# Kernel optimization log

Hardware: AMD Instinct MI355X
Metric: run time of the kernel (lower is better)

The kernel has to match this reference:

```python
import jax, jax.numpy as jnp
import numpy as np

TOTAL_LABELS = 81
MAX_TOTAL_SIZE = 200
SCORE_THRESHOLD = 0.7
IOU_THRESHOLD = 0.5  # tf.image.combined_non_max_suppression default
VARIANCES = jnp.array([0.1, 0.1, 0.2, 0.2], dtype=jnp.float32)
B, N = 4, 1500


def setup_inputs() -> dict:
    key = jax.random.key(0)
    k1, k2, k3, k4, k5 = jax.random.split(key, 5)
    # valid normalized rois (y1,x1,y2,x2) with y1<y2, x1<x2
    ctr = jax.random.uniform(k1, (B, N, 2), minval=0.2, maxval=0.8)
    sz = jax.random.uniform(k2, (B, N, 2), minval=0.05, maxval=0.3)
    roi_bboxes = jnp.concatenate([ctr - 0.5 * sz, ctr + 0.5 * sz], axis=-1).astype(jnp.float32)
    pred_deltas = (0.5 * jax.random.normal(k3, (B, N, TOTAL_LABELS * 4))).astype(jnp.float32)
    # peaked probabilities so a realistic fraction clears score_threshold=0.7
    logits = 4.0 * jax.random.normal(k4, (B, N, TOTAL_LABELS))
    pred_label_probs = jax.nn.softmax(logits, axis=-1).astype(jnp.float32)
    return {"roi_bboxes": roi_bboxes, "pred_deltas": pred_deltas,
            "pred_label_probs": pred_label_probs}


def delta_to_bbox(anchors, deltas):
    # anchors/deltas: [..., 4]; anchors are (y1,x1,y2,x2), deltas (dy,dx,dh,dw)
    h = anchors[..., 2] - anchors[..., 0]
    w = anchors[..., 3] - anchors[..., 1]
    cy = anchors[..., 0] + 0.5 * h
    cx = anchors[..., 1] + 0.5 * w
    bh = jnp.exp(deltas[..., 2]) * h
    bw = jnp.exp(deltas[..., 3]) * w
    bcy = deltas[..., 0] * h + cy
    bcx = deltas[..., 1] * w + cx
    y1 = bcy - 0.5 * bh
    x1 = bcx - 0.5 * bw
    return jnp.stack([y1, x1, y1 + bh, x1 + bw], axis=-1)


def _iou_one_vs_all(box, boxes):
    yy1 = jnp.maximum(box[0], boxes[:, 0])
    xx1 = jnp.maximum(box[1], boxes[:, 1])
    yy2 = jnp.minimum(box[2], boxes[:, 2])
    xx2 = jnp.minimum(box[3], boxes[:, 3])
    inter = jnp.maximum(yy2 - yy1, 0.0) * jnp.maximum(xx2 - xx1, 0.0)
    a1 = (box[2] - box[0]) * (box[3] - box[1])
    a2 = (boxes[:, 2] - boxes[:, 0]) * (boxes[:, 3] - boxes[:, 1])
    union = a1 + a2 - inter
    return jnp.where(union > 0, inter / union, 0.0)


def _greedy_nms(boxes, scores):
    # boxes [N,4], scores [N] -> sel idx [K] (-1 invalid), sel score [K]
    def step(scores_c, _):
        j = jnp.argmax(scores_c)
        s = scores_c[j]
        valid = s > SCORE_THRESHOLD
        iou = _iou_one_vs_all(boxes[j], boxes)
        new_scores = jnp.where(valid & (iou > IOU_THRESHOLD), -jnp.inf, scores_c)
        return new_scores, (jnp.where(valid, j, -1).astype(jnp.int32),
                            jnp.where(valid, s, 0.0))
    _, (idx, sc) = jax.lax.scan(step, scores, None, length=MAX_TOTAL_SIZE)
    return idx, sc


def _decoder_forward(roi_bboxes, pred_deltas, pred_label_probs):
    b, n, L = pred_label_probs.shape
    deltas = pred_deltas.reshape(b, n, L, 4) * VARIANCES
    rois = jnp.broadcast_to(roi_bboxes[:, :, None, :], (b, n, L, 4))
    pred_bboxes = delta_to_bbox(rois, deltas)              # [B,N,L,4]
    labels_map = jnp.argmax(pred_label_probs, axis=-1, keepdims=True)
    scores = jnp.where(labels_map != 0, pred_label_probs, 0.0)  # zero bg boxes
    boxes_cl = jnp.transpose(pred_bboxes, (0, 2, 1, 3))    # [B,L,N,4]
    scores_cl = jnp.transpose(scores, (0, 2, 1))           # [B,L,N]
    idx, sc = jax.vmap(jax.vmap(_greedy_nms))(boxes_cl, scores_cl)  # [B,L,K]
    K = MAX_TOTAL_SIZE
    sel_boxes = jnp.take_along_axis(boxes_cl, jnp.maximum(idx, 0)[..., None], axis=2)
    valid = (idx >= 0)[..., None]
    sel_boxes = jnp.where(valid, jnp.clip(sel_boxes, 0.0, 1.0), 0.0)  # clip_boxes=True
    cls = jnp.broadcast_to(jnp.arange(L, dtype=jnp.float32)[None, :, None], (b, L, K))
    cls = jnp.where(idx >= 0, cls, 0.0)
    flat_scores = sc.reshape(b, L * K)
    flat_boxes = sel_boxes.reshape(b, L * K, 4)
    flat_cls = cls.reshape(b, L * K)
    final_scores, top_i = jax.lax.top_k(flat_scores, MAX_TOTAL_SIZE)
    final_bboxes = jnp.take_along_axis(flat_boxes, top_i[..., None], axis=1)
    final_labels = jnp.take_along_axis(flat_cls, top_i, axis=1)
    return final_bboxes, final_labels, final_scores


def reference(roi_bboxes, pred_deltas, pred_label_probs):
    return _decoder_forward(roi_bboxes, pred_deltas, pred_label_probs)
```

## Files before the change

### kernel.cpp

```cpp
#include <hip/hip_runtime.h>
#include <math.h>

#define NCLS 81
#define KMAX 200
#define NMAX 1536
#define SORT_CAP 2048


__global__ __launch_bounds__(64) void row_scan(
    const float* __restrict__ rois,
    const float* __restrict__ deltas,
    const float* __restrict__ probs,
    int* __restrict__ cand_cls,
    float* __restrict__ cand_sc,
    float4* __restrict__ cand_box,
    int BN) {
  __shared__ float s_p[64 * NCLS];
  const int lane = threadIdx.x;
  const int row0 = blockIdx.x * 64;
  const int nrows = min(64, BN - row0);

  const float* src = probs + (size_t)row0 * NCLS;
  const int tot = nrows * NCLS;
  for (int i = lane; i < tot; i += 64) s_p[i] = src[i];
  __syncthreads();
  if (lane >= nrows) return;

  const int row = row0 + lane;
  const float* pr = s_p + lane * NCLS;
  float maxv = pr[0];
  int arg = 0;
  for (int k = 1; k < NCLS; ++k) {
    const float v = pr[k];
    if (v > maxv) { maxv = v; arg = k; }
  }
  const bool cand = (maxv > 0.7f) && (arg != 0);
  cand_cls[row] = cand ? arg : -1;
  cand_sc[row] = maxv;
  if (cand) {
    const float* r = rois + (size_t)row * 4;
    const float ay1 = r[0], ax1 = r[1], ay2 = r[2], ax2 = r[3];
    const float h = ay2 - ay1, w = ax2 - ax1;
    const float cy = ay1 + 0.5f * h, cx = ax1 + 0.5f * w;
    const float* d = deltas + (size_t)row * (NCLS * 4) + arg * 4;
    const float bh  = expf(d[2] * 0.2f) * h;
    const float bw  = expf(d[3] * 0.2f) * w;
    const float bcy = d[0] * 0.1f * h + cy;
    const float bcx = d[1] * 0.1f * w + cx;
    const float y1 = bcy - 0.5f * bh, x1 = bcx - 0.5f * bw;
    cand_box[row] = make_float4(y1, x1, y1 + bh, x1 + bw);
  }
}

__global__ __launch_bounds__(64) void nms_per_class(
    const int* __restrict__ cand_cls,
    const float* __restrict__ cand_sc,
    const float4* __restrict__ cand_box,
    float* __restrict__ entries,
    int* __restrict__ counts,
    int N) {
  const int bl = blockIdx.x;
  const int b  = bl / NCLS;
  const int l  = bl % NCLS;
  const int lane = threadIdx.x;
  if (l == 0) {
    if (lane == 0) counts[bl] = 0;
    return;
  }

  __shared__ float s_score[NMAX];
  __shared__ float s_box[NMAX][4];
  __shared__ int   s_sel[KMAX];
  __shared__ float s_sel_score[KMAX];

  int m = 0;
  for (int n0 = 0; n0 < N; n0 += 64) {
    const int n = n0 + lane;
    const int c = (n < N) ? cand_cls[b * N + n] : -1;
    const bool cand = (c == l);
    const unsigned long long mask = __ballot(cand);
    if (cand) {
      const int idx = m + __popcll(mask & ((1ull << lane) - 1ull));
      const float4 bx = cand_box[b * N + n];
      s_score[idx]  = cand_sc[b * N + n];
      s_box[idx][0] = bx.x;
      s_box[idx][1] = bx.y;
      s_box[idx][2] = bx.z;
      s_box[idx][3] = bx.w;
    }
    m += __popcll(mask);
  }
  __syncthreads();

  int kept = 0;
  while (kept < KMAX) {
    float best = -1.0f;
    int bi = -1;
    for (int i = lane; i < m; i += 64) {
      const float s = s_score[i];
      if (s > best) { best = s; bi = i; }
    }
    for (int off = 32; off > 0; off >>= 1) {
      const float ob = __shfl_down(best, off);
      const int   oi = __shfl_down(bi, off);
      if (ob > best || (ob == best && (unsigned)oi < (unsigned)bi)) {
        best = ob; bi = oi;
      }
    }
    best = __shfl(best, 0);
    bi   = __shfl(bi, 0);
    if (best <= 0.7f) break;

    if (lane == 0) { s_sel[kept] = bi; s_sel_score[kept] = best; }

    const float by1 = s_box[bi][0], bx1 = s_box[bi][1];
    const float by2 = s_box[bi][2], bx2 = s_box[bi][3];
    const float a1 = (by2 - by1) * (bx2 - bx1);
    for (int i = lane; i < m; i += 64) {
      const float ty1 = s_box[i][0], tx1 = s_box[i][1];
      const float ty2 = s_box[i][2], tx2 = s_box[i][3];
      const float yy1 = fmaxf(by1, ty1), xx1 = fmaxf(bx1, tx1);
      const float yy2 = fminf(by2, ty2), xx2 = fminf(bx2, tx2);
      const float inter = fmaxf(yy2 - yy1, 0.0f) * fmaxf(xx2 - xx1, 0.0f);
      const float a2  = (ty2 - ty1) * (tx2 - tx1);
      const float uni = a1 + a2 - inter;
      const float iou = (uni > 0.0f) ? (inter / uni) : 0.0f;
      if (iou > 0.5f) s_score[i] = -INFINITY;
    }
    kept++;
    __syncthreads();
  }
  __syncthreads();

  if (lane == 0) counts[bl] = kept;
  float* ebase = entries + (size_t)bl * KMAX * 8;
  for (int i = lane; i < kept; i += 64) {
    float* e = ebase + (size_t)i * 8;
    const int ci = s_sel[i];
    e[0] = s_sel_score[i];
    e[1] = fminf(fmaxf(s_box[ci][0], 0.0f), 1.0f);
    e[2] = fminf(fmaxf(s_box[ci][1], 0.0f), 1.0f);
    e[3] = fminf(fmaxf(s_box[ci][2], 0.0f), 1.0f);
    e[4] = fminf(fmaxf(s_box[ci][3], 0.0f), 1.0f);
  }
}

__global__ __launch_bounds__(1024) void topk_per_batch(
    const float* __restrict__ entries,
    const int* __restrict__ counts,
    float* __restrict__ out, int B) {
  const int b   = blockIdx.x;
  const int tid = threadIdx.x;

  __shared__ int s_cnt[NCLS];
  __shared__ int s_off[NCLS];
  __shared__ int s_total, s_M;
  __shared__ unsigned long long s_key[SORT_CAP];

  if (tid < NCLS) s_cnt[tid] = counts[b * NCLS + tid];
  __syncthreads();
  if (tid == 0) {
    int acc = 0;
    for (int l = 0; l < NCLS; ++l) { s_off[l] = acc; acc += s_cnt[l]; }
    s_total = acc;
    int M = 64;
    while (M < acc) M <<= 1;
    s_M = M;
  }
  __syncthreads();
  const int c = s_total;
  const int M = s_M;

  for (int i = tid; i < M; i += 1024) s_key[i] = 0ull;
  __syncthreads();
  for (int j = tid; j < NCLS * KMAX; j += 1024) {
    const int l = j / KMAX, k = j - l * KMAX;
    if (k < s_cnt[l]) {
      const float sc = entries[((size_t)(b * NCLS + l) * KMAX + k) * 8];
      const unsigned sb = __float_as_uint(sc);
      s_key[s_off[l] + k] =
          ((unsigned long long)sb << 32) |
          (unsigned long long)(0xFFFFFFFFu - (unsigned)(l * KMAX + k));
    }
  }
  __syncthreads();

  for (int kk = 2; kk <= M; kk <<= 1) {
    for (int j2 = kk >> 1; j2 > 0; j2 >>= 1) {
      for (int i = tid; i < M; i += 1024) {
        const int ixj = i ^ j2;
        if (ixj > i) {
          const bool up = ((i & kk) == 0);
          const unsigned long long a = s_key[i], bb = s_key[ixj];
          const bool sw = up ? (a < bb) : (a > bb);
          if (sw) { s_key[i] = bb; s_key[ixj] = a; }
        }
      }
      __syncthreads();
    }
  }

  if (tid < KMAX) {
    float sc = 0.0f, lb = 0.0f, b0 = 0.0f, b1 = 0.0f, b2 = 0.0f, b3 = 0.0f;
    if (tid < c) {
      const unsigned long long k = s_key[tid];
      const unsigned fi = 0xFFFFFFFFu - (unsigned)(k & 0xFFFFFFFFull);
      const int l = fi / KMAX, kk2 = fi - l * KMAX;
      const float* e = entries + ((size_t)(b * NCLS + l) * KMAX + kk2) * 8;
      sc = e[0];
      lb = (float)l;
      b0 = e[1]; b1 = e[2]; b2 = e[3]; b3 = e[4];
    }
    float* ob = out + (size_t)b * (KMAX * 4) + (size_t)tid * 4;
    ob[0] = b0; ob[1] = b1; ob[2] = b2; ob[3] = b3;
    const size_t boxes_sz = (size_t)B * KMAX * 4;
    out[boxes_sz + (size_t)b * KMAX + tid] = lb;
    out[boxes_sz + (size_t)B * KMAX + (size_t)b * KMAX + tid] = sc;
  }
}

extern "C" void kernel_launch(void* const* d_in, const int* in_sizes, int n_in,
                              void* d_out, int out_size, void* d_ws, size_t ws_size,
                              hipStream_t stream) {
  const float* rois   = (const float*)d_in[0];
  const float* deltas = (const float*)d_in[1];
  const float* probs  = (const float*)d_in[2];
  float* out = (float*)d_out;

  const int B = 4;
  const int N = in_sizes[0] / (B * 4);
  const int BN = B * N;

  char* ws = (char*)d_ws;
  int*    counts   = (int*)ws;
  float*  entries  = (float*)(ws + 4096);
  int*    cand_cls = (int*)(ws + 2077696);
  float*  cand_sc  = (float*)(ws + 2077696 + 24064);
  float4* cand_box = (float4*)(ws + 2077696 + 24064 + 24064);

  hipLaunchKernelGGL(row_scan, dim3((BN + 63) / 64), dim3(64), 0, stream,
                     rois, deltas, probs, cand_cls, cand_sc, cand_box, BN);
  hipLaunchKernelGGL(nms_per_class, dim3(B * NCLS), dim3(64), 0, stream,
                     cand_cls, cand_sc, cand_box, entries, counts, N);
  hipLaunchKernelGGL(topk_per_batch, dim3(B), dim3(1024), 0, stream,
                     entries, counts, out, B);
}
```

Measured before the change: 51.23 us.

## Fuse row scan, per-class NMS and top-k into one block per batch

Replaces the three-kernel pipeline with a single 1024-thread block per batch. The block computes argmax and decoded boxes into shared memory, then runs per-class greedy NMS with one wave per class using compacted candidate index lists, and finishes with an in-block bitonic sort carrying a payload. This removes two launches and the global round trips through the workspace, at the cost of using only 4 blocks on the whole GPU. The old three-kernel path is kept as a fallback for N above the shared-memory capacity.

```diff
diff --git a/kernel.cpp b/kernel.cpp
--- a/kernel.cpp
+++ b/kernel.cpp
@@ -4,29 +4,244 @@
 #define NCLS 81
 #define KMAX 200
 #define NMAX 1536
+#define WCAP 256
+#define NWAVE 16
 #define SORT_CAP 2048
 
-
-__global__ __launch_bounds__(64) void row_scan(
+__global__ __launch_bounds__(1024) void decoder_fused(
     const float* __restrict__ rois,
     const float* __restrict__ deltas,
     const float* __restrict__ probs,
-    int* __restrict__ cand_cls,
-    float* __restrict__ cand_sc,
-    float4* __restrict__ cand_box,
-    int BN) {
+    float* __restrict__ out, int N, int B) {
+  const int b    = blockIdx.x;
+  const int tid  = threadIdx.x;
+  const int lane = tid & 63;
+  const int wv   = tid >> 6;
+
+  __shared__ int    s_cls[NMAX];
+  __shared__ float  s_sc[NMAX];
+  __shared__ float4 s_box[NMAX];
+  __shared__ int    s_widx[NWAVE * WCAP];
+  __shared__ float  s_wsc[NWAVE * WCAP];
+  __shared__ unsigned long long s_key[SORT_CAP];
+  __shared__ int    s_pay[SORT_CAP];
+  __shared__ float4 s_obox[NMAX];
+  __shared__ int    s_outcnt;
+
+  if (tid == 0) s_outcnt = 0;
+
+  for (int q = 0; q < 2; ++q) {
+    const int s = tid + q * 1024;
+    if (s >= NMAX) break;
+    if (s < N) {
+      const int row = b * N + s;
+      const float* pr = probs + (size_t)row * NCLS;
+      const float4* p4 = (const float4*)pr;
+      float mv = pr[0];
+      int arg = 0;
+#pragma unroll
+      for (int j = 0; j < 20; ++j) {
+        const float4 v = p4[j];
+        const int k0 = j * 4;
+        if (v.x > mv) { mv = v.x; arg = k0; }
+        if (v.y > mv) { mv = v.y; arg = k0 + 1; }
+        if (v.z > mv) { mv = v.z; arg = k0 + 2; }
+        if (v.w > mv) { mv = v.w; arg = k0 + 3; }
+      }
+      const float v80 = pr[80];
+      if (v80 > mv) { mv = v80; arg = 80; }
+      const bool cand = (mv > 0.7f) && (arg != 0);
+      s_cls[s] = cand ? arg : -1;
+      s_sc[s]  = mv;
+      if (cand) {
+        const float4 r4 = *(const float4*)(rois + (size_t)row * 4);
+        const float h = r4.z - r4.x, w = r4.w - r4.y;
+        const float cy = r4.x + 0.5f * h, cx = r4.y + 0.5f * w;
+        const float4 d4 = *(const float4*)(deltas + (size_t)row * (NCLS * 4) + arg * 4);
+        const float bh  = expf(d4.z * 0.2f) * h;
+        const float bw  = expf(d4.w * 0.2f) * w;
+        const float bcy = d4.x * 0.1f * h + cy;
+        const float bcx = d4.y * 0.1f * w + cx;
+        const float y1 = bcy - 0.5f * bh, x1 = bcx - 0.5f * bw;
+        s_box[s] = make_float4(y1, x1, y1 + bh, x1 + bw);
+      }
+    } else {
+      s_cls[s] = -1;
+    }
+  }
+  __syncthreads();
+
+  const int iters = (N + 63) >> 6;
+  int*   widx = s_widx + wv * WCAP;
+  float* wsc  = s_wsc + wv * WCAP;
+
+  for (int l = wv; l < NCLS; l += NWAVE) {
+    if (l == 0) continue;
+    int m = 0;
+    for (int it = 0; it < iters; ++it) {
+      const int idx = (it << 6) + lane;
+      const bool cand = (s_cls[idx] == l);
+      const unsigned long long mask = __ballot(cand);
+      if (cand) {
+        const int p = m + __popcll(mask & ((1ull << lane) - 1ull));
+        if (p < WCAP) widx[p] = idx;
+      }
+      m += __popcll(mask);
+    }
+    if (m == 0) continue;
+    __builtin_amdgcn_wave_barrier();
+
+    if (m <= WCAP) {
+      for (int i = lane; i < m; i += 64) wsc[i] = s_sc[widx[i]];
+      int kept = 0;
+      while (kept < KMAX) {
+        __builtin_amdgcn_wave_barrier();
+        float best = -1.0f; int bi = -1;
+        for (int i = lane; i < m; i += 64) {
+          const float s = wsc[i];
+          if (s > best) { best = s; bi = i; }
+        }
+        for (int off = 32; off > 0; off >>= 1) {
+          const float ob = __shfl_down(best, off);
+          const int   oi = __shfl_down(bi, off);
+          if (ob > best || (ob == best && (unsigned)oi < (unsigned)bi)) {
+            best = ob; bi = oi;
+          }
+        }
+        best = __shfl(best, 0);
+        bi   = __shfl(bi, 0);
+        if (best <= 0.7f) break;
+        const float4 bb = s_box[widx[bi]];
+        const float a1 = (bb.z - bb.x) * (bb.w - bb.y);
+        for (int i = lane; i < m; i += 64) {
+          const float4 tb = s_box[widx[i]];
+          const float yy1 = fmaxf(bb.x, tb.x), xx1 = fmaxf(bb.y, tb.y);
+          const float yy2 = fminf(bb.z, tb.z), xx2 = fminf(bb.w, tb.w);
+          const float inter = fmaxf(yy2 - yy1, 0.0f) * fmaxf(xx2 - xx1, 0.0f);
+          const float a2  = (tb.z - tb.x) * (tb.w - tb.y);
+          const float uni = a1 + a2 - inter;
+          const float iou = (uni > 0.0f) ? (inter / uni) : 0.0f;
+          if (iou > 0.5f) wsc[i] = -INFINITY;
+        }
+        if (lane == 0) {
+          const int slot = atomicAdd(&s_outcnt, 1);
+          const unsigned fi = (unsigned)(l * KMAX + kept);
+          s_key[slot] = ((unsigned long long)__float_as_uint(best) << 32) |
+                        (unsigned long long)(0xFFFFFFFFu - fi);
+          s_pay[slot] = slot;
+          s_obox[slot] = make_float4(
+              fminf(fmaxf(bb.x, 0.0f), 1.0f), fminf(fmaxf(bb.y, 0.0f), 1.0f),
+              fminf(fmaxf(bb.z, 0.0f), 1.0f), fminf(fmaxf(bb.w, 0.0f), 1.0f));
+        }
+        kept++;
+      }
+    } else {
+      int kept = 0;
+      while (kept < KMAX) {
+        __builtin_amdgcn_wave_barrier();
+        float best = -1.0f; int bi = -1;
+        for (int it = 0; it < iters; ++it) {
+          const int idx = (it << 6) + lane;
+          const float s = (s_cls[idx] == l) ? s_sc[idx] : -INFINITY;
+          if (s > best) { best = s; bi = idx; }
+        }
+        for (int off = 32; off > 0; off >>= 1) {
+          const float ob = __shfl_down(best, off);
+          const int   oi = __shfl_down(bi, off);
+          if (ob > best || (ob == best && (unsigned)oi < (unsigned)bi)) {
+            best = ob; bi = oi;
+          }
+        }
+        best = __shfl(best, 0);
+        bi   = __shfl(bi, 0);
+        if (best <= 0.7f) break;
+        const float4 bb = s_box[bi];
+        const float a1 = (bb.z - bb.x) * (bb.w - bb.y);
+        for (int it = 0; it < iters; ++it) {
+          const int idx = (it << 6) + lane;
+          if (s_cls[idx] == l) {
+            const float4 tb = s_box[idx];
+            const float yy1 = fmaxf(bb.x, tb.x), xx1 = fmaxf(bb.y, tb.y);
+            const float yy2 = fminf(bb.z, tb.z), xx2 = fminf(bb.w, tb.w);
+            const float inter = fmaxf(yy2 - yy1, 0.0f) * fmaxf(xx2 - xx1, 0.0f);
+            const float a2  = (tb.z - tb.x) * (tb.w - tb.y);
+            const float uni = a1 + a2 - inter;
+            const float iou = (uni > 0.0f) ? (inter / uni) : 0.0f;
+            if (iou > 0.5f) s_sc[idx] = -INFINITY;
+          }
+        }
+        if (lane == 0) {
+          const int slot = atomicAdd(&s_outcnt, 1);
+          const unsigned fi = (unsigned)(l * KMAX + kept);
+          s_key[slot] = ((unsigned long long)__float_as_uint(best) << 32) |
+                        (unsigned long long)(0xFFFFFFFFu - fi);
+          s_pay[slot] = slot;
+          s_obox[slot] = make_float4(
+              fminf(fmaxf(bb.x, 0.0f), 1.0f), fminf(fmaxf(bb.y, 0.0f), 1.0f),
+              fminf(fmaxf(bb.z, 0.0f), 1.0f), fminf(fmaxf(bb.w, 0.0f), 1.0f));
+        }
+        kept++;
+      }
+    }
+  }
+  __syncthreads();
+
+  const int cnt = s_outcnt;
+  int M = 64;
+  while (M < cnt) M <<= 1;
+  for (int i = tid; i < M; i += 1024)
+    if (i >= cnt) s_key[i] = 0ull;
+  __syncthreads();
+
+  for (int kk = 2; kk <= M; kk <<= 1) {
+    for (int j2 = kk >> 1; j2 > 0; j2 >>= 1) {
+      for (int i = tid; i < M; i += 1024) {
+        const int ixj = i ^ j2;
+        if (ixj > i) {
+          const bool up = ((i & kk) == 0);
+          const unsigned long long a = s_key[i], bb2 = s_key[ixj];
+          const bool sw = up ? (a < bb2) : (a > bb2);
+          if (sw) {
+            s_key[i] = bb2; s_key[ixj] = a;
+            const int t = s_pay[i]; s_pay[i] = s_pay[ixj]; s_pay[ixj] = t;
+          }
+        }
+      }
+      __syncthreads();
+    }
+  }
+
+  if (tid < KMAX) {
+    float sc = 0.0f, lb = 0.0f;
+    float4 bx = make_float4(0.0f, 0.0f, 0.0f, 0.0f);
+    if (tid < cnt) {
+      const unsigned long long k = s_key[tid];
+      sc = __uint_as_float((unsigned)(k >> 32));
+      const unsigned fi = 0xFFFFFFFFu - (unsigned)(k & 0xFFFFFFFFull);
+      lb = (float)(fi / KMAX);
+      bx = s_obox[s_pay[tid]];
+    }
+    float* ob = out + (size_t)b * (KMAX * 4) + (size_t)tid * 4;
+    ob[0] = bx.x; ob[1] = bx.y; ob[2] = bx.z; ob[3] = bx.w;
+    const size_t boxes_sz = (size_t)B * KMAX * 4;
+    out[boxes_sz + (size_t)b * KMAX + tid] = lb;
+    out[boxes_sz + (size_t)B * KMAX + (size_t)b * KMAX + tid] = sc;
+  }
+}
+
+__global__ __launch_bounds__(64) void row_scan_rt(
+    const float* __restrict__ rois, const float* __restrict__ deltas,
+    const float* __restrict__ probs, int* __restrict__ cand_cls,
+    float* __restrict__ cand_sc, float4* __restrict__ cand_box, int BN) {
   __shared__ float s_p[64 * NCLS];
   const int lane = threadIdx.x;
   const int row0 = blockIdx.x * 64;
-  const int nrows = min(64, BN - row0);
-
+  const int tot = (min(64, BN - row0)) * NCLS;
   const float* src = probs + (size_t)row0 * NCLS;
-  const int tot = nrows * NCLS;
   for (int i = lane; i < tot; i += 64) s_p[i] = src[i];
   __syncthreads();
-  if (lane >= nrows) return;
-
   const int row = row0 + lane;
+  if (row >= BN) return;
   const float* pr = s_p + lane * NCLS;
   float maxv = pr[0];
   int arg = 0;
@@ -38,64 +253,49 @@
   cand_cls[row] = cand ? arg : -1;
   cand_sc[row] = maxv;
   if (cand) {
-    const float* r = rois + (size_t)row * 4;
-    const float ay1 = r[0], ax1 = r[1], ay2 = r[2], ax2 = r[3];
-    const float h = ay2 - ay1, w = ax2 - ax1;
-    const float cy = ay1 + 0.5f * h, cx = ax1 + 0.5f * w;
-    const float* d = deltas + (size_t)row * (NCLS * 4) + arg * 4;
-    const float bh  = expf(d[2] * 0.2f) * h;
-    const float bw  = expf(d[3] * 0.2f) * w;
-    const float bcy = d[0] * 0.1f * h + cy;
-    const float bcx = d[1] * 0.1f * w + cx;
+    const float4 r4 = *(const float4*)(rois + (size_t)row * 4);
+    const float h = r4.z - r4.x, w = r4.w - r4.y;
+    const float cy = r4.x + 0.5f * h, cx = r4.y + 0.5f * w;
+    const float4 d4 = *(const float4*)(deltas + (size_t)row * (NCLS * 4) + arg * 4);
+    const float bh  = expf(d4.z * 0.2f) * h;
+    const float bw  = expf(d4.w * 0.2f) * w;
+    const float bcy = d4.x * 0.1f * h + cy;
+    const float bcx = d4.y * 0.1f * w + cx;
     const float y1 = bcy - 0.5f * bh, x1 = bcx - 0.5f * bw;
     cand_box[row] = make_float4(y1, x1, y1 + bh, x1 + bw);
   }
 }
 
-__global__ __launch_bounds__(64) void nms_per_class(
-    const int* __restrict__ cand_cls,
-    const float* __restrict__ cand_sc,
-    const float4* __restrict__ cand_box,
-    float* __restrict__ entries,
-    int* __restrict__ counts,
-    int N) {
+__global__ __launch_bounds__(64) void nms_per_class_rt(
+    const int* __restrict__ cand_cls, const float* __restrict__ cand_sc,
+    const float4* __restrict__ cand_box, float* __restrict__ entries,
+    int* __restrict__ counts, int N) {
   const int bl = blockIdx.x;
   const int b  = bl / NCLS;
   const int l  = bl % NCLS;
   const int lane = threadIdx.x;
-  if (l == 0) {
-    if (lane == 0) counts[bl] = 0;
-    return;
-  }
-
-  __shared__ float s_score[NMAX];
-  __shared__ float s_box[NMAX][4];
+  if (l == 0) { if (lane == 0) counts[bl] = 0; return; }
+
+  __shared__ int   s_idx[8192];
+  __shared__ float s_score[8192];
   __shared__ int   s_sel[KMAX];
   __shared__ float s_sel_score[KMAX];
 
   int m = 0;
   for (int n0 = 0; n0 < N; n0 += 64) {
     const int n = n0 + lane;
-    const int c = (n < N) ? cand_cls[b * N + n] : -1;
-    const bool cand = (c == l);
+    const bool cand = (n < N) && (cand_cls[b * N + n] == l);
     const unsigned long long mask = __ballot(cand);
-    if (cand) {
-      const int idx = m + __popcll(mask & ((1ull << lane) - 1ull));
-      const float4 bx = cand_box[b * N + n];
-      s_score[idx]  = cand_sc[b * N + n];
-      s_box[idx][0] = bx.x;
-      s_box[idx][1] = bx.y;
-      s_box[idx][2] = bx.z;
-      s_box[idx][3] = bx.w;
-    }
+    if (cand) s_idx[m + __popcll(mask & ((1ull << lane) - 1ull))] = n;
     m += __popcll(mask);
   }
+  __syncthreads();
+  for (int i = lane; i < m; i += 64) s_score[i] = cand_sc[b * N + s_idx[i]];
   __syncthreads();
 
   int kept = 0;
   while (kept < KMAX) {
-    float best = -1.0f;
-    int bi = -1;
+    float best = -1.0f; int bi = -1;
     for (int i = lane; i < m; i += 64) {
       const float s = s_score[i];
       if (s > best) { best = s; bi = i; }
@@ -103,26 +303,19 @@
     for (int off = 32; off > 0; off >>= 1) {
       const float ob = __shfl_down(best, off);
       const int   oi = __shfl_down(bi, off);
-      if (ob > best || (ob == best && (unsigned)oi < (unsigned)bi)) {
-        best = ob; bi = oi;
-      }
-    }
-    best = __shfl(best, 0);
-    bi   = __shfl(bi, 0);
+      if (ob > best || (ob == best && (unsigned)oi < (unsigned)bi)) { best = ob; bi = oi; }
+    }
+    best = __shfl(best, 0); bi = __shfl(bi, 0);
     if (best <= 0.7f) break;
-
     if (lane == 0) { s_sel[kept] = bi; s_sel_score[kept] = best; }
-
-    const float by1 = s_box[bi][0], bx1 = s_box[bi][1];
-    const float by2 = s_box[bi][2], bx2 = s_box[bi][3];
-    const float a1 = (by2 - by1) * (bx2 - bx1);
+    const float4 bb = cand_box[b * N + s_idx[bi]];
+    const float a1 = (bb.z - bb.x) * (bb.w - bb.y);
     for (int i = lane; i < m; i += 64) {
-      const float ty1 = s_box[i][0], tx1 = s_box[i][1];
-      const float ty2 = s_box[i][2], tx2 = s_box[i][3];
-      const float yy1 = fmaxf(by1, ty1), xx1 = fmaxf(bx1, tx1);
-      const float yy2 = fminf(by2, ty2), xx2 = fminf(bx2, tx2);
+      const float4 tb = cand_box[b * N + s_idx[i]];
+      const float yy1 = fmaxf(bb.x, tb.x), xx1 = fmaxf(bb.y, tb.y);
+      const float yy2 = fminf(bb.z, tb.z), xx2 = fminf(bb.w, tb.w);
       const float inter = fmaxf(yy2 - yy1, 0.0f) * fmaxf(xx2 - xx1, 0.0f);
-      const float a2  = (ty2 - ty1) * (tx2 - tx1);
+      const float a2  = (tb.z - tb.x) * (tb.w - tb.y);
       const float uni = a1 + a2 - inter;
       const float iou = (uni > 0.0f) ? (inter / uni) : 0.0f;
       if (iou > 0.5f) s_score[i] = -INFINITY;
@@ -136,22 +329,20 @@
   float* ebase = entries + (size_t)bl * KMAX * 8;
   for (int i = lane; i < kept; i += 64) {
     float* e = ebase + (size_t)i * 8;
-    const int ci = s_sel[i];
+    const float4 bb = cand_box[b * N + s_idx[s_sel[i]]];
     e[0] = s_sel_score[i];
-    e[1] = fminf(fmaxf(s_box[ci][0], 0.0f), 1.0f);
-    e[2] = fminf(fmaxf(s_box[ci][1], 0.0f), 1.0f);
-    e[3] = fminf(fmaxf(s_box[ci][2], 0.0f), 1.0f);
-    e[4] = fminf(fmaxf(s_box[ci][3], 0.0f), 1.0f);
+    e[1] = fminf(fmaxf(bb.x, 0.0f), 1.0f);
+    e[2] = fminf(fmaxf(bb.y, 0.0f), 1.0f);
+    e[3] = fminf(fmaxf(bb.z, 0.0f), 1.0f);
+    e[4] = fminf(fmaxf(bb.w, 0.0f), 1.0f);
   }
 }
 
 __global__ __launch_bounds__(1024) void topk_per_batch(
-    const float* __restrict__ entries,
-    const int* __restrict__ counts,
+    const float* __restrict__ entries, const int* __restrict__ counts,
     float* __restrict__ out, int B) {
   const int b   = blockIdx.x;
   const int tid = threadIdx.x;
-
   __shared__ int s_cnt[NCLS];
   __shared__ int s_off[NCLS];
   __shared__ int s_total, s_M;
@@ -170,21 +361,18 @@
   __syncthreads();
   const int c = s_total;
   const int M = s_M;
-
   for (int i = tid; i < M; i += 1024) s_key[i] = 0ull;
   __syncthreads();
   for (int j = tid; j < NCLS * KMAX; j += 1024) {
     const int l = j / KMAX, k = j - l * KMAX;
     if (k < s_cnt[l]) {
       const float sc = entries[((size_t)(b * NCLS + l) * KMAX + k) * 8];
-      const unsigned sb = __float_as_uint(sc);
       s_key[s_off[l] + k] =
-          ((unsigned long long)sb << 32) |
+          ((unsigned long long)__float_as_uint(sc) << 32) |
           (unsigned long long)(0xFFFFFFFFu - (unsigned)(l * KMAX + k));
     }
   }
   __syncthreads();
-
   for (int kk = 2; kk <= M; kk <<= 1) {
     for (int j2 = kk >> 1; j2 > 0; j2 >>= 1) {
       for (int i = tid; i < M; i += 1024) {
@@ -199,7 +387,6 @@
       __syncthreads();
     }
   }
-
   if (tid < KMAX) {
     float sc = 0.0f, lb = 0.0f, b0 = 0.0f, b1 = 0.0f, b2 = 0.0f, b3 = 0.0f;
     if (tid < c) {
@@ -207,8 +394,7 @@
       const unsigned fi = 0xFFFFFFFFu - (unsigned)(k & 0xFFFFFFFFull);
       const int l = fi / KMAX, kk2 = fi - l * KMAX;
       const float* e = entries + ((size_t)(b * NCLS + l) * KMAX + kk2) * 8;
-      sc = e[0];
-      lb = (float)l;
+      sc = e[0]; lb = (float)l;
       b0 = e[1]; b1 = e[2]; b2 = e[3]; b3 = e[4];
     }
     float* ob = out + (size_t)b * (KMAX * 4) + (size_t)tid * 4;
@@ -229,19 +415,23 @@
 
   const int B = 4;
   const int N = in_sizes[0] / (B * 4);
-  const int BN = B * N;
-
-  char* ws = (char*)d_ws;
-  int*    counts   = (int*)ws;
-  float*  entries  = (float*)(ws + 4096);
-  int*    cand_cls = (int*)(ws + 2077696);
-  float*  cand_sc  = (float*)(ws + 2077696 + 24064);
-  float4* cand_box = (float4*)(ws + 2077696 + 24064 + 24064);
-
-  hipLaunchKernelGGL(row_scan, dim3((BN + 63) / 64), dim3(64), 0, stream,
-                     rois, deltas, probs, cand_cls, cand_sc, cand_box, BN);
-  hipLaunchKernelGGL(nms_per_class, dim3(B * NCLS), dim3(64), 0, stream,
-                     cand_cls, cand_sc, cand_box, entries, counts, N);
-  hipLaunchKernelGGL(topk_per_batch, dim3(B), dim3(1024), 0, stream,
-                     entries, counts, out, B);
+
+  if (N <= NMAX) {
+    hipLaunchKernelGGL(decoder_fused, dim3(B), dim3(1024), 0, stream,
+                       rois, deltas, probs, out, N, B);
+  } else {
+    char* ws = (char*)d_ws;
+    int*    counts   = (int*)ws;
+    float*  entries  = (float*)(ws + 4096);
+    int*    cand_cls = (int*)(ws + 4096 + 2100000);
+    float*  cand_sc  = (float*)(ws + 4096 + 2100000 + 64 * (size_t)N);
+    float4* cand_box = (float4*)(ws + 4096 + 2100000 + 128 * (size_t)N);
+    const int BN = B * N;
+    hipLaunchKernelGGL(row_scan_rt, dim3((BN + 63) / 64), dim3(64), 0, stream,
+                       rois, deltas, probs, cand_cls, cand_sc, cand_box, BN);
+    hipLaunchKernelGGL(nms_per_class_rt, dim3(B * NCLS), dim3(64), 0, stream,
+                       cand_cls, cand_sc, cand_box, entries, counts, N);
+    hipLaunchKernelGGL(topk_per_batch, dim3(B), dim3(1024), 0, stream,
+                       entries, counts, out, B);
+  }
 }
```

Result: slower. 95.62 us (+86.7%).
